# Kernel optimization log

Hardware: AMD Instinct MI355X
Metric: run time of the kernel (lower is better)

The kernel has to match this reference:

```python
import jax, jax.numpy as jnp
import numpy as np

NEG_SLOPE = 0.2  # PyG GATv2 default leaky_relu slope

N_NODES = 50000
N_EDGES = 800000
F_IN = 128
HEADS = 4
C_HID = 32   # hidden_dim per head; concat -> 128
C_EMB = 128  # embedding_dim (concat=False, mean over heads)
OUT_DIM = 2


def _glorot(key, shape):
    fan_in, fan_out = shape[0], shape[-1]
    lim = (6.0 / (fan_in + fan_out)) ** 0.5
    return jax.random.uniform(key, shape, jnp.float32, -lim, lim)


def setup_inputs() -> dict:
    key = jax.random.key(0)
    ks = jax.random.split(key, 12)
    x = jax.random.normal(ks[0], (N_NODES, F_IN), jnp.float32)
    edge_index = jax.random.randint(ks[1], (2, N_EDGES), 0, N_NODES, jnp.int64)
    params = {
        # layer 1: F_IN -> (HEADS, C_HID), concat=True
        "Wl1": _glorot(ks[2], (F_IN, HEADS * C_HID)),
        "Wr1": _glorot(ks[3], (F_IN, HEADS * C_HID)),
        "att1": _glorot(ks[4], (HEADS, C_HID)),
        "b1": jnp.zeros((HEADS * C_HID,), jnp.float32),
        # layer 2: HEADS*C_HID -> (HEADS, C_EMB), concat=False (mean)
        "Wl2": _glorot(ks[5], (HEADS * C_HID, HEADS * C_EMB)),
        "Wr2": _glorot(ks[6], (HEADS * C_HID, HEADS * C_EMB)),
        "att2": _glorot(ks[7], (HEADS, C_EMB)),
        "b2": jnp.zeros((C_EMB,), jnp.float32),
        # decoder linear
        "Wo": _glorot(ks[8], (C_EMB, OUT_DIM)),
        "bo": jnp.zeros((OUT_DIM,), jnp.float32),
    }
    return {"x": x, "edge_index": edge_index, **params}


def _gatv2_layer(x, Wl, Wr, att, b, src, dst, n_nodes, concat):
    """GATv2Conv: e_ij = att . leaky_relu(Wl x_j + Wr x_i); segment softmax over dst."""
    H, C = att.shape
    xl = (x @ Wl).reshape(n_nodes, H, C)  # source transform
    xr = (x @ Wr).reshape(n_nodes, H, C)  # target transform
    m = xl[src] + xr[dst]                                  # [E,H,C]
    e = jnp.sum(jax.nn.leaky_relu(m, NEG_SLOPE) * att, axis=-1)  # [E,H]
    # numerically stable segment softmax over edges sharing a dst node
    emax = jax.ops.segment_max(e, dst, num_segments=n_nodes)[dst]
    ex = jnp.exp(e - emax)
    denom = jax.ops.segment_sum(ex, dst, num_segments=n_nodes)[dst]
    alpha = ex / denom                                     # [E,H]
    out = jax.ops.segment_sum(alpha[..., None] * xl[src], dst, num_segments=n_nodes)  # [N,H,C]
    out = out.reshape(n_nodes, H * C) if concat else out.mean(axis=1)
    return out + b


def reference(x, edge_index, Wl1, Wr1, att1, b1, Wl2, Wr2, att2, b2, Wo, bo):
    n = x.shape[0]
    loop = jnp.arange(n, dtype=edge_index.dtype)
    src = jnp.concatenate([edge_index[0], loop])  # PyG adds self-loops by default
    dst = jnp.concatenate([edge_index[1], loop])
    h = _gatv2_layer(x, Wl1, Wr1, att1, b1, src, dst, n, concat=True)
    h = jax.nn.relu(h)
    h = _gatv2_layer(h, Wl2, Wr2, att2, b2, src, dst, n, concat=False)
    out = h @ Wo + bo
    return out, h
```

## Files before the change

kernel.cpp:

```cpp
#include <hip/hip_runtime.h>

#define NEG_SLOPE 0.2f
#define LOG2E 1.44269504088896340736f

typedef unsigned short ushort_t;
typedef unsigned int uint_t;
typedef __attribute__((ext_vector_type(8))) short bf16x8;
typedef __attribute__((ext_vector_type(4))) float f32x4;
typedef __attribute__((ext_vector_type(2))) float f32x2;

__device__ inline float bf2f(ushort_t u) { union { uint_t i; float f; } v; v.i = ((uint_t)u) << 16; return v.f; }
__device__ inline ushort_t f2bf(float f) {
    union { float f; uint_t u; } v; v.f = f;
    uint_t r = v.u + 0x7fffu + ((v.u >> 16) & 1u);
    return (ushort_t)(r >> 16);
}
__device__ inline f32x2 up2v(uint_t w) {
    union { uint_t i; float f; } lo, hi;
    lo.i = w << 16; hi.i = w & 0xFFFF0000u;
    return (f32x2){lo.f, hi.f};
}
__device__ inline f32x2 up2f(uint_t w) {
    union { uint_t i; float f; } lo, hi;
    lo.i = w << 16; hi.i = w;
    return (f32x2){lo.f, hi.f};
}
__device__ inline float ld_f(const void* p, size_t i, int bf) { return bf ? bf2f(((const ushort_t*)p)[i]) : ((const float*)p)[i]; }
__device__ inline ushort_t ld_b(const void* p, size_t i, int bf) { return bf ? ((const ushort_t*)p)[i] : f2bf(((const float*)p)[i]); }
__device__ inline void edge_sd(const int* __restrict__ ei, int e, int E_in, int i64, int& src, int& dst) {
    if (e < E_in) {
        if (i64) { src = ei[2 * (size_t)e]; dst = ei[2 * ((size_t)E_in + e)]; }
        else     { src = ei[e];             dst = ei[(size_t)E_in + e]; }
    } else { src = dst = e - E_in; }
}

template <int CTRL>
__device__ inline float dpp_add(float v) {
    union { float f; int i; } u, r;
    u.f = v;
    r.i = __builtin_amdgcn_update_dpp(0, u.i, CTRL, 0xF, 0xF, true);
    return v + r.f;
}

__device__ inline uint4 ldu4(const ushort_t* __restrict__ base, uint_t boff) {
    return *(const uint4*)((const char*)base + (size_t)boff);
}

__global__ void k_detect(const uint_t* __restrict__ xw, const int* __restrict__ ei, int* flags) {
    __shared__ int cnt;
    if (threadIdx.x == 0) cnt = 0;
    __syncthreads();
    uint_t w = xw[threadIdx.x];
    int eb = (int)((w >> 7) & 0xFFu);
    if (eb >= 113 && eb <= 142) atomicAdd(&cnt, 1);
    __syncthreads();
    if (threadIdx.x == 0) {
        flags[0] = (cnt > 128) ? 1 : 0;
        int z = 0;
        #pragma unroll
        for (int i = 1; i < 16; i += 2) z += (ei[i] == 0) ? 1 : 0;
        flags[1] = (z == 8) ? 1 : 0;
    }
}

__global__ __launch_bounds__(256) void k_prep(const void* __restrict__ x, const void* Wl1, const void* Wr1,
                      const void* att1, const void* b1, const void* Wl2, const void* Wr2,
                      const void* att2, const void* b2, const void* Wo, const void* bo,
                      const int* __restrict__ ei, int E_in, int Etot, int* deg, ushort_t* xb,
                      ushort_t* WTl1, ushort_t* WTr1, ushort_t* WTl2, ushort_t* WTr2,
                      float* att1f, float* b1f, float* att2f, float* b2f, float* Wof, float* bof,
                      int N, int sW1, int sW2, int satt1, int sb1, int satt2, int sb2, int sWo, int sbo,
                      const int* flags) {
    int bf = flags[0];
    long r = (long)blockIdx.x * 256 + threadIdx.x;
    if (r < Etot) {
        int e = (int)r, dst;
        if (e < E_in) dst = flags[1] ? ei[2 * ((size_t)E_in + e)] : ei[(size_t)E_in + e];
        else          dst = e - E_in;
        atomicAdd(&deg[dst], 1);
        return;
    }
    r -= Etot;
    long nx = (long)N * 128;
    if (r < nx) { xb[r] = ld_b(x, r, bf); return; }          r -= nx;
    if (r < sW1) { int n = r >> 7, k = r & 127; WTl1[r] = ld_b(Wl1, (size_t)k * 128 + n, bf); return; } r -= sW1;
    if (r < sW1) { int n = r >> 7, k = r & 127; WTr1[r] = ld_b(Wr1, (size_t)k * 128 + n, bf); return; } r -= sW1;
    if (r < sW2) { int n = r >> 7, k = r & 127; WTl2[r] = ld_b(Wl2, (size_t)k * 512 + n, bf); return; } r -= sW2;
    if (r < sW2) { int n = r >> 7, k = r & 127; WTr2[r] = ld_b(Wr2, (size_t)k * 512 + n, bf); return; } r -= sW2;
    if (r < satt1) { att1f[r] = ld_f(att1, r, bf); return; } r -= satt1;
    if (r < sb1)   { b1f[r]   = ld_f(b1, r, bf);   return; } r -= sb1;
    if (r < satt2) { att2f[r] = ld_f(att2, r, bf); return; } r -= satt2;
    if (r < sb2)   { b2f[r]   = ld_f(b2, r, bf);   return; } r -= sb2;
    if (r < sWo)   { Wof[r]   = ld_f(Wo, r, bf);   return; } r -= sWo;
    if (r < sbo)   { bof[r]   = ld_f(bo, r, bf);   return; }
}

__global__ __launch_bounds__(256) void k_scanA(const int* __restrict__ deg, int* offs, int* bsum, int n) {
    __shared__ int sh[256];
    int t = threadIdx.x;
    int i = blockIdx.x * 256 + t;
    int v = (i < n) ? deg[i] : 0;
    sh[t] = v; __syncthreads();
    #pragma unroll
    for (int off = 1; off < 256; off <<= 1) {
        int u = (t >= off) ? sh[t - off] : 0;
        __syncthreads();
        sh[t] += u; __syncthreads();
    }
    if (i < n) offs[i] = sh[t] - v;
    if (t == 255) bsum[blockIdx.x] = sh[255];
}

__global__ __launch_bounds__(256) void k_scanBC(int* offs, int* cursor, const int* __restrict__ bsum,
                                                int nb, int n) {
    __shared__ int sh[256];
    int t = threadIdx.x;
    int v = (t < nb) ? bsum[t] : 0;
    sh[t] = v; __syncthreads();
    #pragma unroll
    for (int off = 1; off < 256; off <<= 1) {
        int u = (t >= off) ? sh[t - off] : 0;
        __syncthreads();
        sh[t] += u; __syncthreads();
    }
    if (blockIdx.x == 0 && t == 0) { offs[n] = sh[nb - 1]; cursor[n] = sh[nb - 1]; }
    int base = (blockIdx.x > 0) ? sh[blockIdx.x - 1] : 0;
    __syncthreads();
    int i = blockIdx.x * 256 + t;
    if (i < n) {
        int o = offs[i] + base;
        offs[i] = o; cursor[i] = o;
    }
}

__global__ void k_fill(const int* __restrict__ ei, int E_in, int Etot, const int* flags,
                       int* cursor, int* s_src) {
    int e = blockIdx.x * blockDim.x + threadIdx.x;
    if (e >= Etot) return;
    int src, dst; edge_sd(ei, e, E_in, flags[1], src, dst);
    int p = atomicAdd(&cursor[dst], 1);
    s_src[p] = src;
}

#define BPAD 136
template <int NOUT>
__global__ __launch_bounds__(256) void k_gemm2(const ushort_t* __restrict__ X,
                                               const ushort_t* __restrict__ WTl,
                                               const ushort_t* __restrict__ WTr,
                                               ushort_t* __restrict__ Yl,
                                               ushort_t* __restrict__ Yr, int M) {
    __shared__ ushort_t smem[2 * 64 * BPAD];
    const int lane = threadIdx.x & 63, wid = threadIdx.x >> 6;
    const int rt = blockIdx.x * 4 + wid;
    const bool active = rt < (M >> 4);
    const int quad = lane >> 4, lo = lane & 15;

    bf16x8 afr[4];
    if (active) {
        const ushort_t* xrow = X + (size_t)(rt * 16 + lo) * 128 + quad * 8;
        #pragma unroll
        for (int kc = 0; kc < 4; kc++) afr[kc] = *(const bf16x8*)(xrow + kc * 32);
    }

    for (int g = 0; g < NOUT / 64; g++) {
        __syncthreads();
        #pragma unroll
        for (int i = 0; i < 8; i++) {
            int vecid = threadIdx.x * 8 + i;
            int side = vecid >> 10, row = (vecid >> 4) & 63, v = vecid & 15;
            const ushort_t* src = (side ? WTr : WTl) + (size_t)(g * 64 + row) * 128 + v * 8;
            *(bf16x8*)(smem + (size_t)(side * 64 + row) * BPAD + v * 8) = *(const bf16x8*)src;
        }
        __syncthreads();
        if (!active) continue;
        #pragma unroll
        for (int side = 0; side < 2; side++) {
            ushort_t* Y = side ? Yr : Yl;
            f32x4 acc[4];
            #pragma unroll
            for (int nt = 0; nt < 4; nt++) acc[nt] = (f32x4){0.f, 0.f, 0.f, 0.f};
            #pragma unroll
            for (int nt = 0; nt < 4; nt++) {
                const ushort_t* brow = smem + (size_t)(side * 64 + nt * 16 + lo) * BPAD + quad * 8;
                #pragma unroll
                for (int kc = 0; kc < 4; kc++) {
                    bf16x8 b = *(const bf16x8*)(brow + kc * 32);
                    acc[nt] = __builtin_amdgcn_mfma_f32_16x16x32_bf16(afr[kc], b, acc[nt], 0, 0, 0);
                }
            }
            #pragma unroll
            for (int nt = 0; nt < 4; nt++) {
                int col = g * 64 + nt * 16 + lo;
                #pragma unroll
                for (int ri = 0; ri < 4; ri++) {
                    int row = rt * 16 + quad * 4 + ri;
                    Y[(size_t)row * NOUT + col] = f2bf(acc[nt][ri]);
                }
            }
        }
    }
}

__global__ __launch_bounds__(256) void k_l1(const ushort_t* __restrict__ xl,
                                            const ushort_t* __restrict__ xr,
                                            const int* __restrict__ offs,
                                            const int* __restrict__ s_src,
                                            const float* __restrict__ att,
                                            const float* __restrict__ b1,
                                            int n, ushort_t* __restrict__ h1) {
    int lane = threadIdx.x & 63, wid = threadIdx.x >> 6;
    int node = blockIdx.x * 4 + wid;
    if (node >= n) return;
    int slot = lane >> 4, sub = lane & 15;
    int chb = sub * 8;
    uint_t cb = (uint_t)(sub * 16);

    uint4 xw = *(const uint4*)(xr + (size_t)node * 128 + chb);
    f32x2 xv[4] = {up2v(xw.x), up2v(xw.y), up2v(xw.z), up2v(xw.w)};
    f32x2 aL[4];
    #pragma unroll
    for (int j = 0; j < 4; j++) {
        f32x2 a = {att[chb + 2 * j], att[chb + 2 * j + 1]};
        aL[j] = a * (float)LOG2E;
    }

    int o0 = offs[node], o1 = offs[node + 1];
    int last = o1 - 1;
    float s = 0.f;
    f32x2 acc[4] = {{0.f,0.f},{0.f,0.f},{0.f,0.f},{0.f,0.f}};

    int i = o0 + slot;
    uint4 w0 = ldu4(xl, (((uint_t)s_src[min(i, last)])      << 8) + cb);
    uint4 w1 = ldu4(xl, (((uint_t)s_src[min(i + 4, last)])  << 8) + cb);
    uint_t q0 = (((uint_t)s_src[min(i + 8, last)])  << 8) + cb;
    uint_t q1 = (((uint_t)s_src[min(i + 12, last)]) << 8) + cb;

    while (i < o1) {
        uint4 wc = w0;
        w0 = w1;
        w1 = ldu4(xl, q0);
        q0 = q1;
        q1 = (((uint_t)s_src[min(i + 16, last)]) << 8) + cb;
        f32x2 v[4] = {up2v(wc.x), up2v(wc.y), up2v(wc.z), up2v(wc.w)};
        f32x2 es = {0.f, 0.f};
        #pragma unroll
        for (int j = 0; j < 4; j++) {
            f32x2 m = v[j] + xv[j];
            f32x2 l = __builtin_elementwise_max(m, m * NEG_SLOPE);
            es = __builtin_elementwise_fma(aL[j], l, es);
        }
        float e = es.x + es.y;
        e = dpp_add<0xB1>(e);
        e = dpp_add<0x4E>(e);
        float p = __builtin_amdgcn_exp2f(fminf(e, 115.f));
        s += p;
        f32x2 pp = {p, p};
        #pragma unroll
        for (int j = 0; j < 4; j++)
            acc[j] = __builtin_elementwise_fma(pp, v[j], acc[j]);
        i += 4;
    }
    #pragma unroll
    for (int off = 16; off <= 32; off <<= 1) {
        s += __shfl_xor(s, off, 64);
        #pragma unroll
        for (int j = 0; j < 4; j++) {
            f32x2 o = {__shfl_xor(acc[j].x, off, 64), __shfl_xor(acc[j].y, off, 64)};
            acc[j] += o;
        }
    }
    if (slot == 0) {
        float inv = 1.f / s;
        uint_t pk[4];
        #pragma unroll
        for (int j = 0; j < 4; j++) {
            float r0 = fmaxf(fmaf(acc[j].x, inv, b1[chb + 2 * j]),     0.f);
            float r1 = fmaxf(fmaf(acc[j].y, inv, b1[chb + 2 * j + 1]), 0.f);
            pk[j] = (uint_t)f2bf(r0) | ((uint_t)f2bf(r1) << 16);
        }
        *(uint4*)(h1 + (size_t)node * 128 + chb) = make_uint4(pk[0], pk[1], pk[2], pk[3]);
    }
}

__global__ __launch_bounds__(256) void k_l2(const ushort_t* __restrict__ xl,
                                            const ushort_t* __restrict__ xr,
                                            const int* __restrict__ offs,
                                            const int* __restrict__ s_src,
                                            const float* __restrict__ att,
                                            const float* __restrict__ b2,
                                            const float* __restrict__ Wo,
                                            const float* __restrict__ bo,
                                            int n, const int* flags, void* dout) {
    int lane = threadIdx.x & 63, wid = threadIdx.x >> 6;
    int node = blockIdx.x * 4 + wid;
    if (node >= n) return;
    int h = lane >> 4, sub = lane & 15;
    int chb = sub * 8;
    int choff = h * 128 + chb;
    uint_t cb = (uint_t)(choff * 2);

    uint4 xw = *(const uint4*)(xr + (size_t)node * 512 + choff);
    f32x2 xv[4] = {up2v(xw.x), up2v(xw.y), up2v(xw.z), up2v(xw.w)};
    f32x2 aL[4];
    #pragma unroll
    for (int j = 0; j < 4; j++) {
        f32x2 a = {att[choff + 2 * j], att[choff + 2 * j + 1]};
        aL[j] = a * (float)LOG2E;
    }

    int o0 = __builtin_amdgcn_readfirstlane(offs[node]);
    int o1 = __builtin_amdgcn_readfirstlane(offs[node + 1]);
    int cnt = o1 - o0;

    float s = 0.f;
    f32x2 acc[4] = {{0.f,0.f},{0.f,0.f},{0.f,0.f},{0.f,0.f}};
    const char* xlb = (const char*)xl;

    for (int base = 0; base < cnt; base += 64) {
        int m = cnt - base; if (m > 64) m = 64;
        int vidx = s_src[o0 + base + lane];

        auto ROW = [&](int k) -> uint4 {
            int kk = (k < m - 1) ? k : (m - 1);
            int idx = __builtin_amdgcn_readlane(vidx, kk);
            return *(const uint4*)(xlb + (((size_t)(uint_t)idx) << 10) + cb);
        };
        auto PROC = [&](const uint4& w) {
            f32x2 v[4] = {up2f(w.x), up2f(w.y), up2f(w.z), up2f(w.w)};
            f32x2 es = {0.f, 0.f};
            #pragma unroll
            for (int j = 0; j < 4; j++) {
                f32x2 mm = v[j] + xv[j];
                f32x2 l = __builtin_elementwise_max(mm, mm * NEG_SLOPE);
                es = __builtin_elementwise_fma(aL[j], l, es);
            }
            float e = es.x + es.y;
            e = dpp_add<0xB1>(e);
            e = dpp_add<0x4E>(e);
            e = dpp_add<0x141>(e);
            e = dpp_add<0x140>(e);
            float p = __builtin_amdgcn_exp2f(fminf(e, 115.f));
            s += p;
            f32x2 pp = {p, p};
            #pragma unroll
            for (int j = 0; j < 4; j++)
                acc[j] = __builtin_elementwise_fma(pp, v[j], acc[j]);
        };

        uint4 wA = ROW(0), wB = ROW(1), wC = ROW(2), wD = ROW(3);
        int k = 0;
        for (; k + 4 <= m; k += 4) {
            uint4 tA = ROW(k + 4); PROC(wA); wA = tA;
            uint4 tB = ROW(k + 5); PROC(wB); wB = tB;
            uint4 tC = ROW(k + 6); PROC(wC); wC = tC;
            uint4 tD = ROW(k + 7); PROC(wD); wD = tD;
        }
        if (k < m)     PROC(wA);
        if (k + 1 < m) PROC(wB);
        if (k + 2 < m) PROC(wC);
    }

    float inv = 1.f / s;
    f32x2 iv = {inv, inv};
    #pragma unroll
    for (int j = 0; j < 4; j++) acc[j] = acc[j] * iv;
    #pragma unroll
    for (int off = 16; off <= 32; off <<= 1) {
        #pragma unroll
        for (int j = 0; j < 4; j++) {
            f32x2 o = {__shfl_xor(acc[j].x, off, 64), __shfl_xor(acc[j].y, off, 64)};
            acc[j] += o;
        }
    }
    float hm[8];
    #pragma unroll
    for (int j = 0; j < 4; j++) {
        hm[2 * j]     = 0.25f * acc[j].x + b2[chb + 2 * j];
        hm[2 * j + 1] = 0.25f * acc[j].y + b2[chb + 2 * j + 1];
    }

    int bf = flags[0];
    if (h == 0) {
        size_t ob = (size_t)n * 2 + (size_t)node * 128 + chb;
        if (bf) {
            uint_t pk[4];
            #pragma unroll
            for (int j = 0; j < 4; j++)
                pk[j] = (uint_t)f2bf(hm[2 * j]) | ((uint_t)f2bf(hm[2 * j + 1]) << 16);
            *(uint4*)((ushort_t*)dout + ob) = make_uint4(pk[0], pk[1], pk[2], pk[3]);
        } else {
            float* fp = (float*)dout + ob;
            *(float4*)fp       = make_float4(hm[0], hm[1], hm[2], hm[3]);
            *(float4*)(fp + 4) = make_float4(hm[4], hm[5], hm[6], hm[7]);
        }
    }

    float d0 = 0.f, d1 = 0.f;
    #pragma unroll
    for (int c = 0; c < 8; c++) {
        float w0 = Wo[(chb + c) * 2], w1 = Wo[(chb + c) * 2 + 1];
        d0 = fmaf(hm[c], w0, d0);
        d1 = fmaf(hm[c], w1, d1);
    }
    d0 = dpp_add<0xB1>(d0); d0 = dpp_add<0x4E>(d0); d0 = dpp_add<0x141>(d0); d0 = dpp_add<0x140>(d0);
    d1 = dpp_add<0xB1>(d1); d1 = dpp_add<0x4E>(d1); d1 = dpp_add<0x141>(d1); d1 = dpp_add<0x140>(d1);
    if (lane == 0) {
        float r0 = d0 + bo[0], r1 = d1 + bo[1];
        size_t oidx = (size_t)node * 2;
        if (bf) { ((ushort_t*)dout)[oidx] = f2bf(r0); ((ushort_t*)dout)[oidx + 1] = f2bf(r1); }
        else    { ((float*)dout)[oidx]    = r0;       ((float*)dout)[oidx + 1]    = r1; }
    }
}

extern "C" void kernel_launch(void* const* d_in, const int* in_sizes, int n_in,
                              void* d_out, int out_size, void* d_ws, size_t ws_size,
                              hipStream_t stream) {
    const void* x    = d_in[0];
    const int*  ei   = (const int*)d_in[1];
    const void* Wl1  = d_in[2];
    const void* Wr1  = d_in[3];
    const void* att1 = d_in[4];
    const void* b1   = d_in[5];
    const void* Wl2  = d_in[6];
    const void* Wr2  = d_in[7];
    const void* att2 = d_in[8];
    const void* b2   = d_in[9];
    const void* Wo   = d_in[10];
    const void* bo   = d_in[11];

    const int N    = in_sizes[0] / 128;
    const int E_in = in_sizes[1] / 2;
    const int Etot = E_in + N;

    const int sW1 = in_sizes[2], sW2 = in_sizes[6];
    const int satt1 = in_sizes[4], sb1 = in_sizes[5];
    const int satt2 = in_sizes[8], sb2 = in_sizes[9];
    const int sWo = in_sizes[10], sbo = in_sizes[11];

    char* w = (char*)d_ws;
    size_t off = 0;
    auto take = [&](size_t bytes) -> void* {
        void* p = w + off;
        off += (bytes + 255) & ~(size_t)255;
        return p;
    };
    int*      flags  = (int*)take(256);
    ushort_t* xb     = (ushort_t*)take((size_t)N * 128 * sizeof(ushort_t));
    ushort_t* WTl1   = (ushort_t*)take((size_t)sW1 * 2);
    ushort_t* WTr1   = (ushort_t*)take((size_t)sW1 * 2);
    ushort_t* WTl2   = (ushort_t*)take((size_t)sW2 * 2);
    ushort_t* WTr2   = (ushort_t*)take((size_t)sW2 * 2);
    float*    att1f  = (float*)take((size_t)satt1 * 4);
    float*    b1f    = (float*)take((size_t)sb1 * 4);
    float*    att2f  = (float*)take((size_t)satt2 * 4);
    float*    b2f    = (float*)take((size_t)sb2 * 4);
    float*    Wof    = (float*)take((size_t)sWo * 4);
    float*    bof    = (float*)take((size_t)sbo * 4);
    int*      deg    = (int*)take((size_t)N * sizeof(int));
    int*      offs   = (int*)take((size_t)(N + 1) * sizeof(int));
    int*      cursor = (int*)take((size_t)(N + 1) * sizeof(int));
    int*      bsum   = (int*)take(1024);
    int*      s_src  = (int*)take((size_t)(Etot + 64) * sizeof(int));
    ushort_t* h1     = (ushort_t*)take((size_t)N * 128 * sizeof(ushort_t));
    ushort_t* xl1b   = (ushort_t*)take((size_t)N * 128 * sizeof(ushort_t));
    ushort_t* xr1b   = (ushort_t*)take((size_t)N * 128 * sizeof(ushort_t));
    ushort_t* xl2b   = (ushort_t*)take((size_t)N * 512 * sizeof(ushort_t));
    ushort_t* xr2b   = (ushort_t*)take((size_t)N * 512 * sizeof(ushort_t));

    dim3 b256(256);
    const int nb = (N + 255) / 256;

    k_detect<<<1, b256, 0, stream>>>((const uint_t*)x, ei, flags);
    hipMemsetAsync(deg, 0, (size_t)N * sizeof(int), stream);
    hipMemsetAsync(s_src + Etot, 0, 64 * sizeof(int), stream);

    long prep_total = (long)Etot + (long)N * 128 + 2L * sW1 + 2L * sW2
                    + satt1 + sb1 + satt2 + sb2 + sWo + sbo;
    int prep_blocks = (int)((prep_total + 255) / 256);
    k_prep<<<prep_blocks, b256, 0, stream>>>(x, Wl1, Wr1, att1, b1, Wl2, Wr2, att2, b2, Wo, bo,
                                             ei, E_in, Etot, deg, xb, WTl1, WTr1, WTl2, WTr2,
                                             att1f, b1f, att2f, b2f, Wof, bof,
                                             N, sW1, sW2, satt1, sb1, satt2, sb2, sWo, sbo, flags);

    k_scanA<<<nb, b256, 0, stream>>>(deg, offs, bsum, N);
    k_scanBC<<<nb, b256, 0, stream>>>(offs, cursor, bsum, nb, N);
    k_fill<<<(Etot + 255) / 256, b256, 0, stream>>>(ei, E_in, Etot, flags, cursor, s_src);

    dim3 gg((N / 16 + 3) / 4);
    k_gemm2<128><<<gg, b256, 0, stream>>>(xb, WTl1, WTr1, xl1b, xr1b, N);
    k_l1<<<(N + 3) / 4, b256, 0, stream>>>(xl1b, xr1b, offs, s_src, att1f, b1f, N, h1);

    k_gemm2<512><<<gg, b256, 0, stream>>>(h1, WTl2, WTr2, xl2b, xr2b, N);

    k_l2<<<(N + 3) / 4, b256, 0, stream>>>(xl2b, xr2b, offs, s_src, att2f, b2f, Wof, bof, N, flags, d_out);
}
```

Baseline: 431.8 us.

## Make GAT aggregation kernels persistent with next-node prefetch and deeper gather pipeline

Both aggregation kernels now launch a fixed grid of 2048 blocks, and each wave loops over nodes with a grid stride. The loop prefetches the next node's offsets, and in layer 2 also its neighbor index vector, while the current node finishes. This is meant to hide per-node startup latency and cut block launch overhead. Layer 2 also deepens the row-gather software pipeline from 4 to 8 rows in flight and adds a launch_bounds occupancy hint of 6, which raises register pressure and risks spills or lower occupancy.

```diff
diff --git a/kernel.cpp b/kernel.cpp
--- a/kernel.cpp
+++ b/kernel.cpp
@@ -209,14 +209,13 @@
                                             const float* __restrict__ b1,
                                             int n, ushort_t* __restrict__ h1) {
     int lane = threadIdx.x & 63, wid = threadIdx.x >> 6;
-    int node = blockIdx.x * 4 + wid;
-    if (node >= n) return;
+    int gw = blockIdx.x * 4 + wid;
+    if (gw >= n) return;
+    const int W = gridDim.x * 4;
     int slot = lane >> 4, sub = lane & 15;
     int chb = sub * 8;
     uint_t cb = (uint_t)(sub * 16);
 
-    uint4 xw = *(const uint4*)(xr + (size_t)node * 128 + chb);
-    f32x2 xv[4] = {up2v(xw.x), up2v(xw.y), up2v(xw.z), up2v(xw.w)};
     f32x2 aL[4];
     #pragma unroll
     for (int j = 0; j < 4; j++) {
@@ -224,65 +223,79 @@
         aL[j] = a * (float)LOG2E;
     }
 
-    int o0 = offs[node], o1 = offs[node + 1];
-    int last = o1 - 1;
-    float s = 0.f;
-    f32x2 acc[4] = {{0.f,0.f},{0.f,0.f},{0.f,0.f},{0.f,0.f}};
-
-    int i = o0 + slot;
-    uint4 w0 = ldu4(xl, (((uint_t)s_src[min(i, last)])      << 8) + cb);
-    uint4 w1 = ldu4(xl, (((uint_t)s_src[min(i + 4, last)])  << 8) + cb);
-    uint_t q0 = (((uint_t)s_src[min(i + 8, last)])  << 8) + cb;
-    uint_t q1 = (((uint_t)s_src[min(i + 12, last)]) << 8) + cb;
-
-    while (i < o1) {
-        uint4 wc = w0;
-        w0 = w1;
-        w1 = ldu4(xl, q0);
-        q0 = q1;
-        q1 = (((uint_t)s_src[min(i + 16, last)]) << 8) + cb;
-        f32x2 v[4] = {up2v(wc.x), up2v(wc.y), up2v(wc.z), up2v(wc.w)};
-        f32x2 es = {0.f, 0.f};
-        #pragma unroll
-        for (int j = 0; j < 4; j++) {
-            f32x2 m = v[j] + xv[j];
-            f32x2 l = __builtin_elementwise_max(m, m * NEG_SLOPE);
-            es = __builtin_elementwise_fma(aL[j], l, es);
-        }
-        float e = es.x + es.y;
-        e = dpp_add<0xB1>(e);
-        e = dpp_add<0x4E>(e);
-        float p = __builtin_amdgcn_exp2f(fminf(e, 115.f));
-        s += p;
-        f32x2 pp = {p, p};
-        #pragma unroll
-        for (int j = 0; j < 4; j++)
-            acc[j] = __builtin_elementwise_fma(pp, v[j], acc[j]);
-        i += 4;
-    }
-    #pragma unroll
-    for (int off = 16; off <= 32; off <<= 1) {
-        s += __shfl_xor(s, off, 64);
-        #pragma unroll
-        for (int j = 0; j < 4; j++) {
-            f32x2 o = {__shfl_xor(acc[j].x, off, 64), __shfl_xor(acc[j].y, off, 64)};
-            acc[j] += o;
-        }
-    }
-    if (slot == 0) {
-        float inv = 1.f / s;
-        uint_t pk[4];
-        #pragma unroll
-        for (int j = 0; j < 4; j++) {
-            float r0 = fmaxf(fmaf(acc[j].x, inv, b1[chb + 2 * j]),     0.f);
-            float r1 = fmaxf(fmaf(acc[j].y, inv, b1[chb + 2 * j + 1]), 0.f);
-            pk[j] = (uint_t)f2bf(r0) | ((uint_t)f2bf(r1) << 16);
-        }
-        *(uint4*)(h1 + (size_t)node * 128 + chb) = make_uint4(pk[0], pk[1], pk[2], pk[3]);
-    }
-}
-
-__global__ __launch_bounds__(256) void k_l2(const ushort_t* __restrict__ xl,
+    int node = gw;
+    int o0v = offs[node], o1v = offs[node + 1];
+
+    while (node < n) {
+        int nn = node + W;
+        int o0nv = 0, o1nv = 0;
+        if (nn < n) { o0nv = offs[nn]; o1nv = offs[nn + 1]; }
+
+        int o0 = o0v, o1 = o1v;
+        int last = o1 - 1;
+
+        uint4 xw = *(const uint4*)(xr + (size_t)node * 128 + chb);
+        f32x2 xv[4] = {up2v(xw.x), up2v(xw.y), up2v(xw.z), up2v(xw.w)};
+
+        float s = 0.f;
+        f32x2 acc[4] = {{0.f,0.f},{0.f,0.f},{0.f,0.f},{0.f,0.f}};
+
+        int i = o0 + slot;
+        uint4 w0 = ldu4(xl, (((uint_t)s_src[min(i, last)])      << 8) + cb);
+        uint4 w1 = ldu4(xl, (((uint_t)s_src[min(i + 4, last)])  << 8) + cb);
+        uint_t q0 = (((uint_t)s_src[min(i + 8, last)])  << 8) + cb;
+        uint_t q1 = (((uint_t)s_src[min(i + 12, last)]) << 8) + cb;
+
+        while (i < o1) {
+            uint4 wc = w0;
+            w0 = w1;
+            w1 = ldu4(xl, q0);
+            q0 = q1;
+            q1 = (((uint_t)s_src[min(i + 16, last)]) << 8) + cb;
+            f32x2 v[4] = {up2v(wc.x), up2v(wc.y), up2v(wc.z), up2v(wc.w)};
+            f32x2 es = {0.f, 0.f};
+            #pragma unroll
+            for (int j = 0; j < 4; j++) {
+                f32x2 m = v[j] + xv[j];
+                f32x2 l = __builtin_elementwise_max(m, m * NEG_SLOPE);
+                es = __builtin_elementwise_fma(aL[j], l, es);
+            }
+            float e = es.x + es.y;
+            e = dpp_add<0xB1>(e);
+            e = dpp_add<0x4E>(e);
+            float p = __builtin_amdgcn_exp2f(fminf(e, 115.f));
+            s += p;
+            f32x2 pp = {p, p};
+            #pragma unroll
+            for (int j = 0; j < 4; j++)
+                acc[j] = __builtin_elementwise_fma(pp, v[j], acc[j]);
+            i += 4;
+        }
+        #pragma unroll
+        for (int off = 16; off <= 32; off <<= 1) {
+            s += __shfl_xor(s, off, 64);
+            #pragma unroll
+            for (int j = 0; j < 4; j++) {
+                f32x2 o = {__shfl_xor(acc[j].x, off, 64), __shfl_xor(acc[j].y, off, 64)};
+                acc[j] += o;
+            }
+        }
+        if (slot == 0) {
+            float inv = 1.f / s;
+            uint_t pk[4];
+            #pragma unroll
+            for (int j = 0; j < 4; j++) {
+                float r0 = fmaxf(fmaf(acc[j].x, inv, b1[chb + 2 * j]),     0.f);
+                float r1 = fmaxf(fmaf(acc[j].y, inv, b1[chb + 2 * j + 1]), 0.f);
+                pk[j] = (uint_t)f2bf(r0) | ((uint_t)f2bf(r1) << 16);
+            }
+            *(uint4*)(h1 + (size_t)node * 128 + chb) = make_uint4(pk[0], pk[1], pk[2], pk[3]);
+        }
+        node = nn; o0v = o0nv; o1v = o1nv;
+    }
+}
+
+__global__ __launch_bounds__(256, 6) void k_l2(const ushort_t* __restrict__ xl,
                                             const ushort_t* __restrict__ xr,
                                             const int* __restrict__ offs,
                                             const int* __restrict__ s_src,
@@ -292,15 +305,15 @@
                                             const float* __restrict__ bo,
                                             int n, const int* flags, void* dout) {
     int lane = threadIdx.x & 63, wid = threadIdx.x >> 6;
-    int node = blockIdx.x * 4 + wid;
-    if (node >= n) return;
+    int gw = blockIdx.x * 4 + wid;
+    if (gw >= n) return;
+    const int W = gridDim.x * 4;
     int h = lane >> 4, sub = lane & 15;
     int chb = sub * 8;
     int choff = h * 128 + chb;
     uint_t cb = (uint_t)(choff * 2);
-
-    uint4 xw = *(const uint4*)(xr + (size_t)node * 512 + choff);
-    f32x2 xv[4] = {up2v(xw.x), up2v(xw.y), up2v(xw.z), up2v(xw.w)};
+    int bf = flags[0];
+
     f32x2 aL[4];
     #pragma unroll
     for (int j = 0; j < 4; j++) {
@@ -308,107 +321,137 @@
         aL[j] = a * (float)LOG2E;
     }
 
+    const char* xlb = (const char*)xl;
+
+    int node = gw;
     int o0 = __builtin_amdgcn_readfirstlane(offs[node]);
     int o1 = __builtin_amdgcn_readfirstlane(offs[node + 1]);
-    int cnt = o1 - o0;
-
-    float s = 0.f;
-    f32x2 acc[4] = {{0.f,0.f},{0.f,0.f},{0.f,0.f},{0.f,0.f}};
-    const char* xlb = (const char*)xl;
-
-    for (int base = 0; base < cnt; base += 64) {
-        int m = cnt - base; if (m > 64) m = 64;
-        int vidx = s_src[o0 + base + lane];
-
-        auto ROW = [&](int k) -> uint4 {
-            int kk = (k < m - 1) ? k : (m - 1);
-            int idx = __builtin_amdgcn_readlane(vidx, kk);
-            return *(const uint4*)(xlb + (((size_t)(uint_t)idx) << 10) + cb);
-        };
-        auto PROC = [&](const uint4& w) {
-            f32x2 v[4] = {up2f(w.x), up2f(w.y), up2f(w.z), up2f(w.w)};
-            f32x2 es = {0.f, 0.f};
+    int vidx = s_src[o0 + lane];
+
+    while (node < n) {
+        int nn = node + W;
+        int o0nv = 0, o1nv = 0;
+        if (nn < n) { o0nv = offs[nn]; o1nv = offs[nn + 1]; }
+
+        int cnt = o1 - o0;
+
+        uint4 xw = *(const uint4*)(xr + (size_t)node * 512 + choff);
+        f32x2 xv[4] = {up2v(xw.x), up2v(xw.y), up2v(xw.z), up2v(xw.w)};
+
+        float s = 0.f;
+        f32x2 acc[4] = {{0.f,0.f},{0.f,0.f},{0.f,0.f},{0.f,0.f}};
+
+        for (int base = 0; base < cnt; base += 64) {
+            if (base) vidx = s_src[o0 + base + lane];
+            int m = cnt - base; if (m > 64) m = 64;
+
+            auto ROW = [&](int k) -> uint4 {
+                int kk = (k < m - 1) ? k : (m - 1);
+                int idx = __builtin_amdgcn_readlane(vidx, kk);
+                return *(const uint4*)(xlb + (((size_t)(uint_t)idx) << 10) + cb);
+            };
+            auto PROC = [&](const uint4& w) {
+                f32x2 v[4] = {up2f(w.x), up2f(w.y), up2f(w.z), up2f(w.w)};
+                f32x2 es = {0.f, 0.f};
+                #pragma unroll
+                for (int j = 0; j < 4; j++) {
+                    f32x2 mm = v[j] + xv[j];
+                    f32x2 l = __builtin_elementwise_max(mm, mm * NEG_SLOPE);
+                    es = __builtin_elementwise_fma(aL[j], l, es);
+                }
+                float e = es.x + es.y;
+                e = dpp_add<0xB1>(e);
+                e = dpp_add<0x4E>(e);
+                e = dpp_add<0x141>(e);
+                e = dpp_add<0x140>(e);
+                float p = __builtin_amdgcn_exp2f(fminf(e, 115.f));
+                s += p;
+                f32x2 pp = {p, p};
+                #pragma unroll
+                for (int j = 0; j < 4; j++)
+                    acc[j] = __builtin_elementwise_fma(pp, v[j], acc[j]);
+            };
+
+            uint4 wA = ROW(0), wB = ROW(1), wC = ROW(2), wD = ROW(3);
+            uint4 wE = ROW(4), wF = ROW(5), wG = ROW(6), wH = ROW(7);
+            int k = 0;
+            for (; k + 8 <= m; k += 8) {
+                uint4 tA = ROW(k + 8);  PROC(wA); wA = tA;
+                uint4 tB = ROW(k + 9);  PROC(wB); wB = tB;
+                uint4 tC = ROW(k + 10); PROC(wC); wC = tC;
+                uint4 tD = ROW(k + 11); PROC(wD); wD = tD;
+                uint4 tE = ROW(k + 12); PROC(wE); wE = tE;
+                uint4 tF = ROW(k + 13); PROC(wF); wF = tF;
+                uint4 tG = ROW(k + 14); PROC(wG); wG = tG;
+                uint4 tH = ROW(k + 15); PROC(wH); wH = tH;
+            }
+            if (k < m)     PROC(wA);
+            if (k + 1 < m) PROC(wB);
+            if (k + 2 < m) PROC(wC);
+            if (k + 3 < m) PROC(wD);
+            if (k + 4 < m) PROC(wE);
+            if (k + 5 < m) PROC(wF);
+            if (k + 6 < m) PROC(wG);
+        }
+
+        int o0n = 0, o1n = 0, vidxn = 0;
+        if (nn < n) {
+            o0n = __builtin_amdgcn_readfirstlane(o0nv);
+            o1n = __builtin_amdgcn_readfirstlane(o1nv);
+            vidxn = s_src[o0n + lane];
+        }
+
+        float inv = 1.f / s;
+        f32x2 iv = {inv, inv};
+        #pragma unroll
+        for (int j = 0; j < 4; j++) acc[j] = acc[j] * iv;
+        #pragma unroll
+        for (int off = 16; off <= 32; off <<= 1) {
             #pragma unroll
             for (int j = 0; j < 4; j++) {
-                f32x2 mm = v[j] + xv[j];
-                f32x2 l = __builtin_elementwise_max(mm, mm * NEG_SLOPE);
-                es = __builtin_elementwise_fma(aL[j], l, es);
-            }
-            float e = es.x + es.y;
-            e = dpp_add<0xB1>(e);
-            e = dpp_add<0x4E>(e);
-            e = dpp_add<0x141>(e);
-            e = dpp_add<0x140>(e);
-            float p = __builtin_amdgcn_exp2f(fminf(e, 115.f));
-            s += p;
-            f32x2 pp = {p, p};
-            #pragma unroll
-            for (int j = 0; j < 4; j++)
-                acc[j] = __builtin_elementwise_fma(pp, v[j], acc[j]);
-        };
-
-        uint4 wA = ROW(0), wB = ROW(1), wC = ROW(2), wD = ROW(3);
-        int k = 0;
-        for (; k + 4 <= m; k += 4) {
-            uint4 tA = ROW(k + 4); PROC(wA); wA = tA;
-            uint4 tB = ROW(k + 5); PROC(wB); wB = tB;
-            uint4 tC = ROW(k + 6); PROC(wC); wC = tC;
-            uint4 tD = ROW(k + 7); PROC(wD); wD = tD;
-        }
-        if (k < m)     PROC(wA);
-        if (k + 1 < m) PROC(wB);
-        if (k + 2 < m) PROC(wC);
-    }
-
-    float inv = 1.f / s;
-    f32x2 iv = {inv, inv};
-    #pragma unroll
-    for (int j = 0; j < 4; j++) acc[j] = acc[j] * iv;
-    #pragma unroll
-    for (int off = 16; off <= 32; off <<= 1) {
+                f32x2 o = {__shfl_xor(acc[j].x, off, 64), __shfl_xor(acc[j].y, off, 64)};
+                acc[j] += o;
+            }
+        }
+        float hm[8];
         #pragma unroll
         for (int j = 0; j < 4; j++) {
-            f32x2 o = {__shfl_xor(acc[j].x, off, 64), __shfl_xor(acc[j].y, off, 64)};
-            acc[j] += o;
-        }
-    }
-    float hm[8];
-    #pragma unroll
-    for (int j = 0; j < 4; j++) {
-        hm[2 * j]     = 0.25f * acc[j].x + b2[chb + 2 * j];
-        hm[2 * j + 1] = 0.25f * acc[j].y + b2[chb + 2 * j + 1];
-    }
-
-    int bf = flags[0];
-    if (h == 0) {
-        size_t ob = (size_t)n * 2 + (size_t)node * 128 + chb;
-        if (bf) {
-            uint_t pk[4];
-            #pragma unroll
-            for (int j = 0; j < 4; j++)
-                pk[j] = (uint_t)f2bf(hm[2 * j]) | ((uint_t)f2bf(hm[2 * j + 1]) << 16);
-            *(uint4*)((ushort_t*)dout + ob) = make_uint4(pk[0], pk[1], pk[2], pk[3]);
-        } else {
-            float* fp = (float*)dout + ob;
-            *(float4*)fp       = make_float4(hm[0], hm[1], hm[2], hm[3]);
-            *(float4*)(fp + 4) = make_float4(hm[4], hm[5], hm[6], hm[7]);
-        }
-    }
-
-    float d0 = 0.f, d1 = 0.f;
-    #pragma unroll
-    for (int c = 0; c < 8; c++) {
-        float w0 = Wo[(chb + c) * 2], w1 = Wo[(chb + c) * 2 + 1];
-        d0 = fmaf(hm[c], w0, d0);
-        d1 = fmaf(hm[c], w1, d1);
-    }
-    d0 = dpp_add<0xB1>(d0); d0 = dpp_add<0x4E>(d0); d0 = dpp_add<0x141>(d0); d0 = dpp_add<0x140>(d0);
-    d1 = dpp_add<0xB1>(d1); d1 = dpp_add<0x4E>(d1); d1 = dpp_add<0x141>(d1); d1 = dpp_add<0x140>(d1);
-    if (lane == 0) {
-        float r0 = d0 + bo[0], r1 = d1 + bo[1];
-        size_t oidx = (size_t)node * 2;
-        if (bf) { ((ushort_t*)dout)[oidx] = f2bf(r0); ((ushort_t*)dout)[oidx + 1] = f2bf(r1); }
-        else    { ((float*)dout)[oidx]    = r0;       ((float*)dout)[oidx + 1]    = r1; }
+            hm[2 * j]     = 0.25f * acc[j].x + b2[chb + 2 * j];
+            hm[2 * j + 1] = 0.25f * acc[j].y + b2[chb + 2 * j + 1];
+        }
+
+        if (h == 0) {
+            size_t ob = (size_t)n * 2 + (size_t)node * 128 + chb;
+            if (bf) {
+                uint_t pk[4];
+                #pragma unroll
+                for (int j = 0; j < 4; j++)
+                    pk[j] = (uint_t)f2bf(hm[2 * j]) | ((uint_t)f2bf(hm[2 * j + 1]) << 16);
+                *(uint4*)((ushort_t*)dout + ob) = make_uint4(pk[0], pk[1], pk[2], pk[3]);
+            } else {
+                float* fp = (float*)dout + ob;
+                *(float4*)fp       = make_float4(hm[0], hm[1], hm[2], hm[3]);
+                *(float4*)(fp + 4) = make_float4(hm[4], hm[5], hm[6], hm[7]);
+            }
+        }
+
+        float d0 = 0.f, d1 = 0.f;
+        #pragma unroll
+        for (int c = 0; c < 8; c++) {
+            float w0 = Wo[(chb + c) * 2], w1 = Wo[(chb + c) * 2 + 1];
+            d0 = fmaf(hm[c], w0, d0);
+            d1 = fmaf(hm[c], w1, d1);
+        }
+        d0 = dpp_add<0xB1>(d0); d0 = dpp_add<0x4E>(d0); d0 = dpp_add<0x141>(d0); d0 = dpp_add<0x140>(d0);
+        d1 = dpp_add<0xB1>(d1); d1 = dpp_add<0x4E>(d1); d1 = dpp_add<0x141>(d1); d1 = dpp_add<0x140>(d1);
+        if (lane == 0) {
+            float r0 = d0 + bo[0], r1 = d1 + bo[1];
+            size_t oidx = (size_t)node * 2;
+            if (bf) { ((ushort_t*)dout)[oidx] = f2bf(r0); ((ushort_t*)dout)[oidx + 1] = f2bf(r1); }
+            else    { ((float*)dout)[oidx]    = r0;       ((float*)dout)[oidx + 1]    = r1; }
+        }
+
+        node = nn; o0 = o0n; o1 = o1n; vidx = vidxn;
     }
 }
 
@@ -488,9 +531,9 @@
 
     dim3 gg((N / 16 + 3) / 4);
     k_gemm2<128><<<gg, b256, 0, stream>>>(xb, WTl1, WTr1, xl1b, xr1b, N);
-    k_l1<<<(N + 3) / 4, b256, 0, stream>>>(xl1b, xr1b, offs, s_src, att1f, b1f, N, h1);
+    k_l1<<<2048, b256, 0, stream>>>(xl1b, xr1b, offs, s_src, att1f, b1f, N, h1);
 
     k_gemm2<512><<<gg, b256, 0, stream>>>(h1, WTl2, WTr2, xl2b, xr2b, N);
 
-    k_l2<<<(N + 3) / 4, b256, 0, stream>>>(xl2b, xr2b, offs, s_src, att2f, b2f, Wof, bof, N, flags, d_out);
-}
+    k_l2<<<2048, b256, 0, stream>>>(xl2b, xr2b, offs, s_src, att2f, b2f, Wof, bof, N, flags, d_out);
+}
```

Measured after the change: 899.3 us. 2.08x slower.

## Make layer-2 aggregation persistent with next-node index prefetch; guard layer-1 tail loads

Applied to the files above, without the earlier changes.

Layer-2 aggregation becomes a persistent grid-stride kernel with 2048 blocks, so each wave loops over nodes. While processing the current node it prefetches the next node's CSR offsets and first source indices, hiding the latency of the dependent index loads. Layer 1 replaces clamped duplicate tail loads with predicated loads, so gathers past the segment end are skipped. The persistent grid may reduce occupancy or leave load imbalance compared with one wave per node.

```diff
diff --git a/kernel.cpp b/kernel.cpp
--- a/kernel.cpp
+++ b/kernel.cpp
@@ -225,22 +225,23 @@
     }
 
     int o0 = offs[node], o1 = offs[node + 1];
-    int last = o1 - 1;
     float s = 0.f;
     f32x2 acc[4] = {{0.f,0.f},{0.f,0.f},{0.f,0.f},{0.f,0.f}};
 
     int i = o0 + slot;
-    uint4 w0 = ldu4(xl, (((uint_t)s_src[min(i, last)])      << 8) + cb);
-    uint4 w1 = ldu4(xl, (((uint_t)s_src[min(i + 4, last)])  << 8) + cb);
-    uint_t q0 = (((uint_t)s_src[min(i + 8, last)])  << 8) + cb;
-    uint_t q1 = (((uint_t)s_src[min(i + 12, last)]) << 8) + cb;
+    uint_t q0 = 0, q1 = 0;
+    uint4 w0 = {0,0,0,0}, w1 = {0,0,0,0};
+    if (i < o1)      w0 = ldu4(xl, (((uint_t)s_src[i])      << 8) + cb);
+    if (i + 4 < o1)  w1 = ldu4(xl, (((uint_t)s_src[i + 4])  << 8) + cb);
+    if (i + 8 < o1)  q0 = (((uint_t)s_src[i + 8])  << 8) + cb;
+    if (i + 12 < o1) q1 = (((uint_t)s_src[i + 12]) << 8) + cb;
 
     while (i < o1) {
         uint4 wc = w0;
         w0 = w1;
-        w1 = ldu4(xl, q0);
+        if (i + 8 < o1) w1 = ldu4(xl, q0);
         q0 = q1;
-        q1 = (((uint_t)s_src[min(i + 16, last)]) << 8) + cb;
+        if (i + 16 < o1) q1 = (((uint_t)s_src[i + 16]) << 8) + cb;
         f32x2 v[4] = {up2v(wc.x), up2v(wc.y), up2v(wc.z), up2v(wc.w)};
         f32x2 es = {0.f, 0.f};
         #pragma unroll
@@ -292,15 +293,15 @@
                                             const float* __restrict__ bo,
                                             int n, const int* flags, void* dout) {
     int lane = threadIdx.x & 63, wid = threadIdx.x >> 6;
-    int node = blockIdx.x * 4 + wid;
-    if (node >= n) return;
+    int gw = blockIdx.x * 4 + wid;
+    if (gw >= n) return;
+    const int W = gridDim.x * 4;
     int h = lane >> 4, sub = lane & 15;
     int chb = sub * 8;
     int choff = h * 128 + chb;
     uint_t cb = (uint_t)(choff * 2);
-
-    uint4 xw = *(const uint4*)(xr + (size_t)node * 512 + choff);
-    f32x2 xv[4] = {up2v(xw.x), up2v(xw.y), up2v(xw.z), up2v(xw.w)};
+    int bf = flags[0];
+
     f32x2 aL[4];
     #pragma unroll
     for (int j = 0; j < 4; j++) {
@@ -308,107 +309,128 @@
         aL[j] = a * (float)LOG2E;
     }
 
+    const char* xlb = (const char*)xl;
+
+    int node = gw;
     int o0 = __builtin_amdgcn_readfirstlane(offs[node]);
     int o1 = __builtin_amdgcn_readfirstlane(offs[node + 1]);
-    int cnt = o1 - o0;
-
-    float s = 0.f;
-    f32x2 acc[4] = {{0.f,0.f},{0.f,0.f},{0.f,0.f},{0.f,0.f}};
-    const char* xlb = (const char*)xl;
-
-    for (int base = 0; base < cnt; base += 64) {
-        int m = cnt - base; if (m > 64) m = 64;
-        int vidx = s_src[o0 + base + lane];
-
-        auto ROW = [&](int k) -> uint4 {
-            int kk = (k < m - 1) ? k : (m - 1);
-            int idx = __builtin_amdgcn_readlane(vidx, kk);
-            return *(const uint4*)(xlb + (((size_t)(uint_t)idx) << 10) + cb);
-        };
-        auto PROC = [&](const uint4& w) {
-            f32x2 v[4] = {up2f(w.x), up2f(w.y), up2f(w.z), up2f(w.w)};
-            f32x2 es = {0.f, 0.f};
+    int vidx = s_src[o0 + lane];
+
+    while (node < n) {
+        int nn = node + W;
+        int o0nv = 0, o1nv = 0;
+        if (nn < n) { o0nv = offs[nn]; o1nv = offs[nn + 1]; }
+
+        int cnt = o1 - o0;
+
+        uint4 xw = *(const uint4*)(xr + (size_t)node * 512 + choff);
+        f32x2 xv[4] = {up2v(xw.x), up2v(xw.y), up2v(xw.z), up2v(xw.w)};
+
+        float s = 0.f;
+        f32x2 acc[4] = {{0.f,0.f},{0.f,0.f},{0.f,0.f},{0.f,0.f}};
+
+        for (int base = 0; base < cnt; base += 64) {
+            if (base) vidx = s_src[o0 + base + lane];
+            int m = cnt - base; if (m > 64) m = 64;
+
+            auto ROW = [&](int k) -> uint4 {
+                int kk = (k < m - 1) ? k : (m - 1);
+                int idx = __builtin_amdgcn_readlane(vidx, kk);
+                return *(const uint4*)(xlb + (((size_t)(uint_t)idx) << 10) + cb);
+            };
+            auto PROC = [&](const uint4& w) {
+                f32x2 v[4] = {up2f(w.x), up2f(w.y), up2f(w.z), up2f(w.w)};
+                f32x2 es = {0.f, 0.f};
+                #pragma unroll
+                for (int j = 0; j < 4; j++) {
+                    f32x2 mm = v[j] + xv[j];
+                    f32x2 l = __builtin_elementwise_max(mm, mm * NEG_SLOPE);
+                    es = __builtin_elementwise_fma(aL[j], l, es);
+                }
+                float e = es.x + es.y;
+                e = dpp_add<0xB1>(e);
+                e = dpp_add<0x4E>(e);
+                e = dpp_add<0x141>(e);
+                e = dpp_add<0x140>(e);
+                float p = __builtin_amdgcn_exp2f(fminf(e, 115.f));
+                s += p;
+                f32x2 pp = {p, p};
+                #pragma unroll
+                for (int j = 0; j < 4; j++)
+                    acc[j] = __builtin_elementwise_fma(pp, v[j], acc[j]);
+            };
+
+            uint4 wA = ROW(0), wB = ROW(1), wC = ROW(2), wD = ROW(3);
+            int k = 0;
+            for (; k + 4 <= m; k += 4) {
+                uint4 tA = ROW(k + 4); PROC(wA); wA = tA;
+                uint4 tB = ROW(k + 5); PROC(wB); wB = tB;
+                uint4 tC = ROW(k + 6); PROC(wC); wC = tC;
+                uint4 tD = ROW(k + 7); PROC(wD); wD = tD;
+            }
+            if (k < m)     PROC(wA);
+            if (k + 1 < m) PROC(wB);
+            if (k + 2 < m) PROC(wC);
+        }
+
+        int o0n = 0, o1n = 0, vidxn = 0;
+        if (nn < n) {
+            o0n = __builtin_amdgcn_readfirstlane(o0nv);
+            o1n = __builtin_amdgcn_readfirstlane(o1nv);
+            vidxn = s_src[o0n + lane];
+        }
+
+        float inv = 1.f / s;
+        f32x2 iv = {inv, inv};
+        #pragma unroll
+        for (int j = 0; j < 4; j++) acc[j] = acc[j] * iv;
+        #pragma unroll
+        for (int off = 16; off <= 32; off <<= 1) {
             #pragma unroll
             for (int j = 0; j < 4; j++) {
-                f32x2 mm = v[j] + xv[j];
-                f32x2 l = __builtin_elementwise_max(mm, mm * NEG_SLOPE);
-                es = __builtin_elementwise_fma(aL[j], l, es);
+                f32x2 o = {__shfl_xor(acc[j].x, off, 64), __shfl_xor(acc[j].y, off, 64)};
+                acc[j] += o;
             }
-            float e = es.x + es.y;
-            e = dpp_add<0xB1>(e);
-            e = dpp_add<0x4E>(e);
-            e = dpp_add<0x141>(e);
-            e = dpp_add<0x140>(e);
-            float p = __builtin_amdgcn_exp2f(fminf(e, 115.f));
-            s += p;
-            f32x2 pp = {p, p};
-            #pragma unroll
-            for (int j = 0; j < 4; j++)
-                acc[j] = __builtin_elementwise_fma(pp, v[j], acc[j]);
-        };
-
-        uint4 wA = ROW(0), wB = ROW(1), wC = ROW(2), wD = ROW(3);
-        int k = 0;
-        for (; k + 4 <= m; k += 4) {
-            uint4 tA = ROW(k + 4); PROC(wA); wA = tA;
-            uint4 tB = ROW(k + 5); PROC(wB); wB = tB;
-            uint4 tC = ROW(k + 6); PROC(wC); wC = tC;
-            uint4 tD = ROW(k + 7); PROC(wD); wD = tD;
-        }
-        if (k < m)     PROC(wA);
-        if (k + 1 < m) PROC(wB);
-        if (k + 2 < m) PROC(wC);
-    }
-
-    float inv = 1.f / s;
-    f32x2 iv = {inv, inv};
-    #pragma unroll
-    for (int j = 0; j < 4; j++) acc[j] = acc[j] * iv;
-    #pragma unroll
-    for (int off = 16; off <= 32; off <<= 1) {
+        }
+        float hm[8];
         #pragma unroll
         for (int j = 0; j < 4; j++) {
-            f32x2 o = {__shfl_xor(acc[j].x, off, 64), __shfl_xor(acc[j].y, off, 64)};
-            acc[j] += o;
-        }
-    }
-    float hm[8];
-    #pragma unroll
-    for (int j = 0; j < 4; j++) {
-        hm[2 * j]     = 0.25f * acc[j].x + b2[chb + 2 * j];
-        hm[2 * j + 1] = 0.25f * acc[j].y + b2[chb + 2 * j + 1];
-    }
-
-    int bf = flags[0];
-    if (h == 0) {
-        size_t ob = (size_t)n * 2 + (size_t)node * 128 + chb;
-        if (bf) {
-            uint_t pk[4];
-            #pragma unroll
-            for (int j = 0; j < 4; j++)
-                pk[j] = (uint_t)f2bf(hm[2 * j]) | ((uint_t)f2bf(hm[2 * j + 1]) << 16);
-            *(uint4*)((ushort_t*)dout + ob) = make_uint4(pk[0], pk[1], pk[2], pk[3]);
-        } else {
-            float* fp = (float*)dout + ob;
-            *(float4*)fp       = make_float4(hm[0], hm[1], hm[2], hm[3]);
-            *(float4*)(fp + 4) = make_float4(hm[4], hm[5], hm[6], hm[7]);
-        }
-    }
-
-    float d0 = 0.f, d1 = 0.f;
-    #pragma unroll
-    for (int c = 0; c < 8; c++) {
-        float w0 = Wo[(chb + c) * 2], w1 = Wo[(chb + c) * 2 + 1];
-        d0 = fmaf(hm[c], w0, d0);
-        d1 = fmaf(hm[c], w1, d1);
-    }
-    d0 = dpp_add<0xB1>(d0); d0 = dpp_add<0x4E>(d0); d0 = dpp_add<0x141>(d0); d0 = dpp_add<0x140>(d0);
-    d1 = dpp_add<0xB1>(d1); d1 = dpp_add<0x4E>(d1); d1 = dpp_add<0x141>(d1); d1 = dpp_add<0x140>(d1);
-    if (lane == 0) {
-        float r0 = d0 + bo[0], r1 = d1 + bo[1];
-        size_t oidx = (size_t)node * 2;
-        if (bf) { ((ushort_t*)dout)[oidx] = f2bf(r0); ((ushort_t*)dout)[oidx + 1] = f2bf(r1); }
-        else    { ((float*)dout)[oidx]    = r0;       ((float*)dout)[oidx + 1]    = r1; }
+            hm[2 * j]     = 0.25f * acc[j].x + b2[chb + 2 * j];
+            hm[2 * j + 1] = 0.25f * acc[j].y + b2[chb + 2 * j + 1];
+        }
+
+        if (h == 0) {
+            size_t ob = (size_t)n * 2 + (size_t)node * 128 + chb;
+            if (bf) {
+                uint_t pk[4];
+                #pragma unroll
+                for (int j = 0; j < 4; j++)
+                    pk[j] = (uint_t)f2bf(hm[2 * j]) | ((uint_t)f2bf(hm[2 * j + 1]) << 16);
+                *(uint4*)((ushort_t*)dout + ob) = make_uint4(pk[0], pk[1], pk[2], pk[3]);
+            } else {
+                float* fp = (float*)dout + ob;
+                *(float4*)fp       = make_float4(hm[0], hm[1], hm[2], hm[3]);
+                *(float4*)(fp + 4) = make_float4(hm[4], hm[5], hm[6], hm[7]);
+            }
+        }
+
+        float d0 = 0.f, d1 = 0.f;
+        #pragma unroll
+        for (int c = 0; c < 8; c++) {
+            float w0 = Wo[(chb + c) * 2], w1 = Wo[(chb + c) * 2 + 1];
+            d0 = fmaf(hm[c], w0, d0);
+            d1 = fmaf(hm[c], w1, d1);
+        }
+        d0 = dpp_add<0xB1>(d0); d0 = dpp_add<0x4E>(d0); d0 = dpp_add<0x141>(d0); d0 = dpp_add<0x140>(d0);
+        d1 = dpp_add<0xB1>(d1); d1 = dpp_add<0x4E>(d1); d1 = dpp_add<0x141>(d1); d1 = dpp_add<0x140>(d1);
+        if (lane == 0) {
+            float r0 = d0 + bo[0], r1 = d1 + bo[1];
+            size_t oidx = (size_t)node * 2;
+            if (bf) { ((ushort_t*)dout)[oidx] = f2bf(r0); ((ushort_t*)dout)[oidx + 1] = f2bf(r1); }
+            else    { ((float*)dout)[oidx]    = r0;       ((float*)dout)[oidx + 1]    = r1; }
+        }
+
+        node = nn; o0 = o0n; o1 = o1n; vidx = vidxn;
     }
 }
 
@@ -492,5 +514,5 @@
 
     k_gemm2<512><<<gg, b256, 0, stream>>>(h1, WTl2, WTr2, xl2b, xr2b, N);
 
-    k_l2<<<(N + 3) / 4, b256, 0, stream>>>(xl2b, xr2b, offs, s_src, att2f, b2f, Wof, bof, N, flags, d_out);
-}
+    k_l2<<<2048, b256, 0, stream>>>(xl2b, xr2b, offs, s_src, att2f, b2f, Wof, bof, N, flags, d_out);
+}
```

Result: no change. 436.2 us (+1.0%).
